# Performance work log

Hardware: AMD Instinct MI355X
Metric: run time of the kernel (lower is better)

## Reference

```python
import jax, jax.numpy as jnp
import numpy as np

EPS = 1e-6
H = 12  # num_heads


def _rms(x, w):
    return x / jnp.sqrt(jnp.mean(x * x, axis=-1, keepdims=True) + EPS) * w


def _rot_half(x):
    x1, x2 = jnp.split(x, 2, axis=-1)
    return jnp.concatenate([-x2, x1], axis=-1)


def _rope(t, cos, sin):
    # t: [B,H,N,hd]; cos/sin: [N,hd] broadcast
    return t * cos + _rot_half(t) * sin


def setup_inputs() -> dict:
    key = jax.random.key(0)
    B, N, D, Nc = 1, 2048, 768, 16
    hd = D // H
    mh = 4 * D
    ks = jax.random.split(key, 16)
    s = 0.02
    g = lambda k, shape, sc=1.0: jax.random.normal(k, shape, dtype=jnp.float32) * sc
    # real RoPE tables (half-duplicated layout to match rotate_half)
    inv = 1.0 / (10000.0 ** (np.arange(hd // 2, dtype=np.float64) / (hd // 2)))
    ang = np.arange(N, dtype=np.float64)[:, None] * inv[None, :]
    cos = jnp.asarray(np.concatenate([np.cos(ang), np.cos(ang)], -1), dtype=jnp.float32)
    sin = jnp.asarray(np.concatenate([np.sin(ang), np.sin(ang)], -1), dtype=jnp.float32)
    return {
        'x': g(ks[0], (B, N, D)),
        'c': g(ks[1], (B, D)),
        'cond': g(ks[2], (B, Nc, D)),
        'rope_cos': cos,
        'rope_sin': sin,
        'norm1_w': jnp.ones((D,), jnp.float32),
        'norm2_w': jnp.ones((D,), jnp.float32),
        'norm3_w': jnp.ones((D,), jnp.float32),
        'cond_norm_w': jnp.ones((D,), jnp.float32),
        'sa_qkv_w': g(ks[3], (3 * D, D), s),
        'sa_proj_w': g(ks[4], (D, D), s),
        'sa_proj_b': jnp.zeros((D,), jnp.float32),
        'sa_qn_w': jnp.ones((hd,), jnp.float32),
        'sa_kn_w': jnp.ones((hd,), jnp.float32),
        'ca_q_w': g(ks[5], (D, D), s),
        'ca_k_w': g(ks[6], (D, D), s),
        'ca_v_w': g(ks[7], (D, D), s),
        'ca_proj_w': g(ks[8], (D, D), s),
        'ca_proj_b': jnp.zeros((D,), jnp.float32),
        'ca_qn_w': jnp.ones((hd,), jnp.float32),
        'ca_kn_w': jnp.ones((hd,), jnp.float32),
        'mlp_w1': g(ks[9], (mh, D), s),
        'mlp_w2': g(ks[10], (D, mh), s),
        'mlp_w3': g(ks[11], (mh, D), s),
        'ada_w': g(ks[12], (9 * D, D), s),
        'ada_b': jnp.zeros((9 * D,), jnp.float32),
    }


def reference(x, c, cond, rope_cos, rope_sin, norm1_w, norm2_w, norm3_w, cond_norm_w,
              sa_qkv_w, sa_proj_w, sa_proj_b, sa_qn_w, sa_kn_w,
              ca_q_w, ca_k_w, ca_v_w, ca_proj_w, ca_proj_b, ca_qn_w, ca_kn_w,
              mlp_w1, mlp_w2, mlp_w3, ada_w, ada_b):
    B, N, D = x.shape
    hd = D // H
    scale = hd ** -0.5

    # adaLN modulation: SiLU(c) -> Linear -> 9 chunks of [B, D]
    mod = jax.nn.silu(c) @ ada_w.T + ada_b
    (sh_msa, sc_msa, g_msa, sh_ca, sc_ca, g_ca,
     sh_mlp, sc_mlp, g_mlp) = jnp.split(mod, 9, axis=1)

    def modulate(h, sh, sc):
        return h * (1.0 + sc[:, None, :]) + sh[:, None, :]

    # ---- self-attention with QK-norm + RoPE ----
    h = modulate(_rms(x, norm1_w), sh_msa, sc_msa)
    qkv = (h @ sa_qkv_w.T).reshape(B, N, 3, H, hd).transpose(2, 0, 3, 1, 4)  # [3,B,H,N,hd]
    q, k, v = qkv[0], qkv[1], qkv[2]
    q = _rope(_rms(q, sa_qn_w), rope_cos, rope_sin)
    k = _rope(_rms(k, sa_kn_w), rope_cos, rope_sin)
    attn = jax.nn.softmax(jnp.einsum('bhid,bhjd->bhij', q, k) * scale, axis=-1)
    o = jnp.einsum('bhij,bhjd->bhid', attn, v).transpose(0, 2, 1, 3).reshape(B, N, D)
    x = x + g_msa[:, None, :] * (o @ sa_proj_w.T + sa_proj_b)

    # ---- cross-attention (RoPE on q only) ----
    h = modulate(_rms(x, norm2_w), sh_ca, sc_ca)
    cn = _rms(cond, cond_norm_w)
    Nc = cond.shape[1]
    q = (h @ ca_q_w.T).reshape(B, N, H, hd).transpose(0, 2, 1, 3)
    k = (cn @ ca_k_w.T).reshape(B, Nc, H, hd).transpose(0, 2, 1, 3)
    v = (cn @ ca_v_w.T).reshape(B, Nc, H, hd).transpose(0, 2, 1, 3)
    q = _rope(_rms(q, ca_qn_w), rope_cos, rope_sin)
    k = _rms(k, ca_kn_w)
    attn = jax.nn.softmax(jnp.einsum('bhid,bhjd->bhij', q, k) * scale, axis=-1)
    o = jnp.einsum('bhij,bhjd->bhid', attn, v).transpose(0, 2, 1, 3).reshape(B, N, D)
    x = x + g_ca[:, None, :] * (o @ ca_proj_w.T + ca_proj_b)

    # ---- SwiGLU MLP ----
    h = modulate(_rms(x, norm3_w), sh_mlp, sc_mlp)
    x = x + g_mlp[:, None, :] * ((jax.nn.silu(h @ mlp_w1.T) * (h @ mlp_w3.T)) @ mlp_w2.T)
    return x
```

## Files before the change

### kernel.cpp

```cpp
#include <hip/hip_runtime.h>

typedef unsigned short u16;
typedef unsigned int u32;
typedef __attribute__((ext_vector_type(8))) short s16x8;
typedef __attribute__((ext_vector_type(4))) float f32x4;
typedef __attribute__((ext_vector_type(4))) int i32x4;

#define PS 1572864

#define OFF_SAQKV  0
#define OFF_SAPROJ 1769472
#define OFF_CAQ    2359296
#define OFF_CAPROJ 2949120
#define OFF_W1     3538944
#define OFF_W2     5898240
#define OFF_W3     8257536

static __device__ __forceinline__ float bf2f(u16 u) {
    return __uint_as_float(((u32)u) << 16);
}
static __device__ __forceinline__ u16 f2bf(float f) {
    u32 x = __float_as_uint(f);
    return (u16)((x + 0x7fffu + ((x >> 16) & 1u)) >> 16);
}
static __device__ __forceinline__ i32x4 pack8(float4 a, float4 b) {
    u32 p0 = (u32)f2bf(a.x) | ((u32)f2bf(a.y) << 16);
    u32 p1 = (u32)f2bf(a.z) | ((u32)f2bf(a.w) << 16);
    u32 p2 = (u32)f2bf(b.x) | ((u32)f2bf(b.y) << 16);
    u32 p3 = (u32)f2bf(b.z) | ((u32)f2bf(b.w) << 16);
    return (i32x4){(int)p0, (int)p1, (int)p2, (int)p3};
}
static __device__ __forceinline__ float wave_sum(float v) {
#pragma unroll
    for (int off = 32; off > 0; off >>= 1) v += __shfl_xor(v, off);
    return v;
}
static __device__ __forceinline__ void gload16(const void* g, void* l) {
    __builtin_amdgcn_global_load_lds((const __attribute__((address_space(1))) void*)g,
                                     (__attribute__((address_space(3))) void*)l, 16, 0, 0);
}

__global__ __launch_bounds__(256) void cvt_ada(const float* __restrict__ s0,
                                               const float* __restrict__ s1,
                                               const float* __restrict__ s2,
                                               const float* __restrict__ s3,
                                               const float* __restrict__ s4,
                                               const float* __restrict__ s5,
                                               const float* __restrict__ s6,
                                               u16* __restrict__ wall,
                                               const float* __restrict__ c,
                                               const float* __restrict__ adaw,
                                               const float* __restrict__ adab,
                                               float* __restrict__ mod,
                                               const float* __restrict__ cond,
                                               const float* __restrict__ cnw,
                                               const float* __restrict__ cakw,
                                               const float* __restrict__ cavw,
                                               const float* __restrict__ caknw,
                                               float* __restrict__ kca,
                                               float* __restrict__ vca) {
    const int bid = blockIdx.x;
    const int tid = threadIdx.x;
    if (bid < 5184) {
        int u = bid * 256 + tid;
        const float* src;
        int rel;
        if (u < 221184)       { src = s0; rel = u; }
        else if (u < 294912)  { src = s1; rel = u - 221184; }
        else if (u < 368640)  { src = s2; rel = u - 294912; }
        else if (u < 442368)  { src = s3; rel = u - 368640; }
        else if (u < 737280)  { src = s4; rel = u - 442368; }
        else if (u < 1032192) { src = s5; rel = u - 737280; }
        else                  { src = s6; rel = u - 1032192; }
        float4 a = *(const float4*)(src + (size_t)rel * 8);
        float4 b = *(const float4*)(src + (size_t)rel * 8 + 4);
        *(i32x4*)(wall + (size_t)u * 8) = pack8(a, b);
    } else if (bid < 6912) {
        int wid = (bid - 5184) * 4 + (tid >> 6);
        int lane = tid & 63;
        float sum = 0.f;
#pragma unroll
        for (int i = 0; i < 12; ++i) {
            float cv = c[i * 64 + lane];
            cv = cv / (1.f + __expf(-cv));
            sum += cv * adaw[(size_t)wid * 768 + i * 64 + lane];
        }
        sum = wave_sum(sum);
        if (lane == 0) mod[wid] = sum + adab[wid];
    } else {
        int b = bid - 6912;
        int which = b / 192;
        int rem = b % 192;
        int rrow = rem / 12, h = rem % 12;
        int w = tid >> 6, lane = tid & 63;
        __shared__ float kvsh[64];
        float cv[12];
        float ss = 0.f;
#pragma unroll
        for (int i = 0; i < 12; ++i) {
            cv[i] = cond[(size_t)rrow * 768 + i * 64 + lane];
            ss += cv[i] * cv[i];
        }
        ss = wave_sum(ss);
        float rn = rsqrtf(ss * (1.f / 768.f) + 1e-6f);
#pragma unroll
        for (int i = 0; i < 12; ++i) cv[i] = cv[i] * rn * cnw[i * 64 + lane];
        const float* Wm = which ? cavw : cakw;
#pragma unroll
        for (int j = 0; j < 16; ++j) {
            int ocol = h * 64 + w * 16 + j;
            float d = 0.f;
#pragma unroll
            for (int i = 0; i < 12; ++i)
                d += cv[i] * Wm[(size_t)ocol * 768 + i * 64 + lane];
            d = wave_sum(d);
            if (lane == 0) kvsh[w * 16 + j] = d;
        }
        __syncthreads();
        if (tid < 64) {
            float v = kvsh[lane];
            if (which == 0) {
                float sk = wave_sum(v * v);
                v = v * rsqrtf(sk * (1.f / 64.f) + 1e-6f) * caknw[lane];
                kca[(size_t)rrow * 768 + h * 64 + lane] = v;
            } else {
                vca[(size_t)rrow * 768 + h * 64 + lane] = v;
            }
        }
    }
}

__global__ __launch_bounds__(256) void rms_mod(const float* __restrict__ x,
                                               const float* __restrict__ w,
                                               const float* __restrict__ mod, int chunk,
                                               u16* __restrict__ out) {
    const int row = blockIdx.x;
    const int tid = threadIdx.x;
    const float* xr = x + (size_t)row * 768;
    float v0 = xr[tid], v1 = xr[256 + tid], v2 = xr[512 + tid];
    float ss = wave_sum(v0 * v0 + v1 * v1 + v2 * v2);
    __shared__ float red[4];
    if ((tid & 63) == 0) red[tid >> 6] = ss;
    __syncthreads();
    float rn = rsqrtf((red[0] + red[1] + red[2] + red[3]) * (1.f / 768.f) + 1e-6f);
    const float* sh = mod + chunk * 768;
    const float* sc = sh + 768;
    u16* orow = out + (size_t)row * 768;
    orow[tid]       = f2bf(v0 * rn * w[tid]       * (1.f + sc[tid])       + sh[tid]);
    orow[256 + tid] = f2bf(v1 * rn * w[256 + tid] * (1.f + sc[256 + tid]) + sh[256 + tid]);
    orow[512 + tid] = f2bf(v2 * rn * w[512 + tid] * (1.f + sc[512 + tid]) + sh[512 + tid]);
}

__global__ __launch_bounds__(256) void gemm_qkv(const u16* __restrict__ A,
                                                const u16* __restrict__ Wb,
                                                u16* __restrict__ qkvb,
                                                u16* __restrict__ vT,
                                                const float* __restrict__ qnw,
                                                const float* __restrict__ knw,
                                                const float* __restrict__ cosT,
                                                const float* __restrict__ sinT,
                                                int C, int R, int nxc) {
    constexpr int K = 768, N = 2304;
    __shared__ __align__(16) char smem[33792];
    u16 (*As)[128 * 32] = (u16(*)[128 * 32])smem;
    u16 (*Bs)[64 * 32] = (u16(*)[64 * 32])(smem + 16384);
    const int tid = threadIdx.x;
    const int lane = tid & 63;
    const int w = tid >> 6;
    const int wr = w >> 1, wc = w & 1;
    const int sub = blockIdx.x;
    const int xcd = sub & 7, idx = sub >> 3;
    const int cx = xcd % nxc, cy = xcd / nxc;
    const int col0 = (cx * C + idx % C) << 6;
    const int row0 = (cy * R + idx / C) << 7;

    const int r0u = tid >> 2, s0u = (tid & 3) ^ (r0u & 3);
    const int r1u = (tid + 256) >> 2, s1u = (tid & 3) ^ (r1u & 3);
    const u16* a0 = A + (size_t)(row0 + r0u) * K + s0u * 8;
    const u16* a1 = A + (size_t)(row0 + r1u) * K + s1u * 8;
    const u16* b0 = Wb + (size_t)(col0 + r0u) * K + s0u * 8;

    f32x4 acc[4][2];
#pragma unroll
    for (int m = 0; m < 4; ++m)
#pragma unroll
        for (int n = 0; n < 2; ++n) acc[m][n] = (f32x4){0.f, 0.f, 0.f, 0.f};

    const int nt = K >> 5;
    int cur = 0;
#define QKV_STAGE(buf, k0)                                  \
    {                                                       \
        char* ad = (char*)As[buf] + w * 1024;               \
        char* bd = (char*)Bs[buf] + w * 1024;               \
        gload16(a0 + (k0), ad);                             \
        gload16(a1 + (k0), ad + 4096);                      \
        gload16(b0 + (k0), bd);                             \
    }
    QKV_STAGE(0, 0)
    for (int t = 0; t < nt; ++t) {
        __syncthreads();
        if (t + 1 < nt) QKV_STAGE(cur ^ 1, (t + 1) << 5)
        s16x8 af[4], bfv[2];
#pragma unroll
        for (int m = 0; m < 4; ++m) {
            int ra = wr * 64 + m * 16 + (lane & 15);
            int u = (lane >> 4) ^ (ra & 3);
            af[m] = *(const s16x8*)((const char*)As[cur] + ra * 64 + u * 16);
        }
#pragma unroll
        for (int n = 0; n < 2; ++n) {
            int cb = wc * 32 + n * 16 + (lane & 15);
            int u = (lane >> 4) ^ (cb & 3);
            bfv[n] = *(const s16x8*)((const char*)Bs[cur] + cb * 64 + u * 16);
        }
#pragma unroll
        for (int m = 0; m < 4; ++m)
#pragma unroll
            for (int n = 0; n < 2; ++n)
                acc[m][n] = __builtin_amdgcn_mfma_f32_16x16x32_bf16(af[m], bfv[n], acc[m][n], 0, 0, 0);
        cur ^= 1;
    }
#undef QKV_STAGE
    __syncthreads();

    const int region = col0 / 768;
    const int h = (col0 % 768) >> 6;
    if (region < 2) {
        float (*T)[66] = (float(*)[66])smem;
#pragma unroll
        for (int m = 0; m < 4; ++m)
#pragma unroll
            for (int n = 0; n < 2; ++n)
#pragma unroll
                for (int i = 0; i < 4; ++i)
                    T[wr * 64 + m * 16 + (lane >> 4) * 4 + i]
                     [wc * 32 + n * 16 + (lane & 15)] = acc[m][n][i];
        __syncthreads();
        const float* wv = region ? knw : qnw;
        const int rl = tid >> 1, half = (tid & 1) * 32;
        float ss = 0.f;
#pragma unroll
        for (int d = 0; d < 32; ++d) {
            float v = T[rl][half + d];
            ss += v * v;
        }
        ss += __shfl_xor(ss, 1);
        float rn = rsqrtf(ss * (1.f / 64.f) + 1e-6f);
        const int ng = row0 + rl;
        u16* orow = qkvb + (size_t)ng * N + col0;
        const float* cr = cosT + ng * 64;
        const float* sr = sinT + ng * 64;
#pragma unroll
        for (int d = 0; d < 32; ++d) {
            int dd = half + d;
            float vn = T[rl][dd] * rn * wv[dd];
            float pt = T[rl][dd ^ 32] * rn * wv[dd ^ 32];
            float rot = (dd < 32) ? -pt : pt;
            orow[dd] = f2bf(vn * cr[dd] + rot * sr[dd]);
        }
    } else {
        u16 (*Tb)[66] = (u16(*)[66])smem;
#pragma unroll
        for (int m = 0; m < 4; ++m)
#pragma unroll
            for (int n = 0; n < 2; ++n)
#pragma unroll
                for (int i = 0; i < 4; ++i) {
                    int rl = wr * 64 + m * 16 + (lane >> 4) * 4 + i;
                    int dd = wc * 32 + n * 16 + (lane & 15);
                    u16 b = f2bf(acc[m][n][i]);
                    qkvb[(size_t)(row0 + rl) * N + col0 + dd] = b;
                    Tb[rl][dd] = b;
                }
        __syncthreads();
        u16* dst = vT + (size_t)h * 131072 + (size_t)lane * 2048 + row0 + w * 32;
#pragma unroll
        for (int g = 0; g < 4; ++g) {
            s16x8 o;
#pragma unroll
            for (int e = 0; e < 8; ++e) o[e] = (short)Tb[w * 32 + g * 8 + e][lane];
            *(s16x8*)(dst + g * 8) = o;
        }
    }
}

__global__ __launch_bounds__(256) void gemm_sk4(const u16* __restrict__ A,
                                                const u16* __restrict__ Wb,
                                                int M, int N, int K,
                                                u16* __restrict__ pz,
                                                int C, int R, int nxc,
                                                int nsub, int kslice) {
    __shared__ __align__(16) u16 As[2][128 * 32];
    __shared__ __align__(16) u16 Bs[2][64 * 32];
    const int tid = threadIdx.x;
    const int lane = tid & 63;
    const int w = tid >> 6;
    const int wr = w >> 1, wc = w & 1;
    const int sub = blockIdx.x % nsub;
    const int z = blockIdx.x / nsub;
    const int xcd = sub & 7, idx = sub >> 3;
    const int cx = xcd % nxc, cy = xcd / nxc;
    const int col0 = (cx * C + idx % C) << 6;
    const int row0 = (cy * R + idx / C) << 7;
    const int kbase = z * kslice;

    const int r0u = tid >> 2, s0u = (tid & 3) ^ (r0u & 3);
    const int r1u = (tid + 256) >> 2, s1u = (tid & 3) ^ (r1u & 3);
    const u16* a0 = A + (size_t)(row0 + r0u) * K + kbase + s0u * 8;
    const u16* a1 = A + (size_t)(row0 + r1u) * K + kbase + s1u * 8;
    const u16* b0 = Wb + (size_t)(col0 + r0u) * K + kbase + s0u * 8;

    f32x4 acc[4][2];
#pragma unroll
    for (int m = 0; m < 4; ++m)
#pragma unroll
        for (int n = 0; n < 2; ++n) acc[m][n] = (f32x4){0.f, 0.f, 0.f, 0.f};

    const int nt = kslice >> 5;
    int cur = 0;
#define SK_STAGE(buf, k0)                                   \
    {                                                       \
        char* ad = (char*)As[buf] + w * 1024;               \
        char* bd = (char*)Bs[buf] + w * 1024;               \
        gload16(a0 + (k0), ad);                             \
        gload16(a1 + (k0), ad + 4096);                      \
        gload16(b0 + (k0), bd);                             \
    }
    SK_STAGE(0, 0)
    for (int t = 0; t < nt; ++t) {
        __syncthreads();
        if (t + 1 < nt) SK_STAGE(cur ^ 1, (t + 1) << 5)
        s16x8 af[4], bfv[2];
#pragma unroll
        for (int m = 0; m < 4; ++m) {
            int ra = wr * 64 + m * 16 + (lane & 15);
            int u = (lane >> 4) ^ (ra & 3);
            af[m] = *(const s16x8*)((const char*)As[cur] + ra * 64 + u * 16);
        }
#pragma unroll
        for (int n = 0; n < 2; ++n) {
            int cb = wc * 32 + n * 16 + (lane & 15);
            int u = (lane >> 4) ^ (cb & 3);
            bfv[n] = *(const s16x8*)((const char*)Bs[cur] + cb * 64 + u * 16);
        }
#pragma unroll
        for (int m = 0; m < 4; ++m)
#pragma unroll
            for (int n = 0; n < 2; ++n)
                acc[m][n] = __builtin_amdgcn_mfma_f32_16x16x32_bf16(af[m], bfv[n], acc[m][n], 0, 0, 0);
        cur ^= 1;
    }
#undef SK_STAGE
    u16* po = pz + (size_t)z * PS;
#pragma unroll
    for (int m = 0; m < 4; ++m)
#pragma unroll
        for (int n = 0; n < 2; ++n)
#pragma unroll
            for (int i = 0; i < 4; ++i) {
                int r = row0 + wr * 64 + m * 16 + (lane >> 4) * 4 + i;
                int cc = col0 + wc * 32 + n * 16 + (lane & 15);
                po[(size_t)r * N + cc] = f2bf(acc[m][n][i]);
            }
}

template <int MODE>
__global__ __launch_bounds__(256) void comb4(const u16* __restrict__ pz,
                                             const float* __restrict__ resid,
                                             const float* __restrict__ gate,
                                             const float* __restrict__ bias,
                                             float* __restrict__ outf) {
    int base = (blockIdx.x * 256 + threadIdx.x) * 8;
    int col = base % 768;
    s16x8 p0 = *(const s16x8*)(pz + base);
    s16x8 p1 = *(const s16x8*)(pz + PS + base);
    s16x8 p2 = *(const s16x8*)(pz + 2 * PS + base);
    s16x8 p3 = *(const s16x8*)(pz + 3 * PS + base);
    float o[8];
#pragma unroll
    for (int e = 0; e < 8; ++e) {
        float s = (bf2f((u16)p0[e]) + bf2f((u16)p1[e])) +
                  (bf2f((u16)p2[e]) + bf2f((u16)p3[e]));
        if constexpr (MODE == 0) {
            o[e] = s;
        } else {
            float bb = bias ? bias[col + e] : 0.f;
            o[e] = resid[base + e] + gate[col + e] * (s + bb);
        }
    }
    *(float4*)(outf + base) = (float4){o[0], o[1], o[2], o[3]};
    *(float4*)(outf + base + 4) = (float4){o[4], o[5], o[6], o[7]};
}

__global__ __launch_bounds__(256) void comb_rms(const u16* __restrict__ pz,
                                                const float* __restrict__ resid,
                                                const float* __restrict__ gate,
                                                const float* __restrict__ bias,
                                                const float* __restrict__ mod, int chunk,
                                                const float* __restrict__ w,
                                                float* __restrict__ outf,
                                                u16* __restrict__ outb) {
    const int row = blockIdx.x;
    const int tid = threadIdx.x;
    float val[3];
    float ss = 0.f;
#pragma unroll
    for (int j = 0; j < 3; ++j) {
        int col = tid + j * 256;
        size_t ix = (size_t)row * 768 + col;
        float s = (bf2f(pz[ix]) + bf2f(pz[PS + ix])) +
                  (bf2f(pz[2 * PS + ix]) + bf2f(pz[3 * PS + ix]));
        float bb = bias ? bias[col] : 0.f;
        float v = resid[ix] + gate[col] * (s + bb);
        val[j] = v;
        ss += v * v;
        outf[ix] = v;
    }
    ss = wave_sum(ss);
    __shared__ float red[4];
    if ((tid & 63) == 0) red[tid >> 6] = ss;
    __syncthreads();
    float rn = rsqrtf((red[0] + red[1] + red[2] + red[3]) * (1.f / 768.f) + 1e-6f);
    const float* sh = mod + chunk * 768;
    const float* sc = sh + 768;
#pragma unroll
    for (int j = 0; j < 3; ++j) {
        int col = tid + j * 256;
        size_t ix = (size_t)row * 768 + col;
        outb[ix] = f2bf(val[j] * rn * w[col] * (1.f + sc[col]) + sh[col]);
    }
}

__global__ __launch_bounds__(256) void ca_fused(const u16* __restrict__ pz,
                                                const float* __restrict__ qnw,
                                                const float* __restrict__ cosT,
                                                const float* __restrict__ sinT,
                                                const float* __restrict__ kca,
                                                const float* __restrict__ vca,
                                                u16* __restrict__ obuf) {
    int wid = blockIdx.x * 4 + (threadIdx.x >> 6);
    int lane = threadIdx.x & 63;
    int n = wid / 12, h = wid % 12;
    size_t ix = (size_t)n * 768 + h * 64 + lane;
    float v = (bf2f(pz[ix]) + bf2f(pz[PS + ix])) +
              (bf2f(pz[2 * PS + ix]) + bf2f(pz[3 * PS + ix]));
    float ss = wave_sum(v * v);
    float vn = v * rsqrtf(ss * (1.f / 64.f) + 1e-6f) * qnw[lane];
    float part = __shfl_xor(vn, 32);
    float rot = (lane < 32) ? -part : part;
    float qd = (vn * cosT[n * 64 + lane] + rot * sinT[n * 64 + lane]) * 0.125f;
    float s[16];
#pragma unroll
    for (int j = 0; j < 16; ++j)
        s[j] = wave_sum(qd * kca[(size_t)j * 768 + h * 64 + lane]);
    float mm = s[0];
#pragma unroll
    for (int j = 1; j < 16; ++j) mm = fmaxf(mm, s[j]);
    float l = 0.f;
#pragma unroll
    for (int j = 0; j < 16; ++j) { s[j] = __expf(s[j] - mm); l += s[j]; }
    float od = 0.f;
#pragma unroll
    for (int j = 0; j < 16; ++j) od += s[j] * vca[(size_t)j * 768 + h * 64 + lane];
    obuf[ix] = f2bf(od / l);
}

__global__ __launch_bounds__(256) void gemm_w13(const u16* __restrict__ A,
                                                const u16* __restrict__ W1,
                                                const u16* __restrict__ W3,
                                                int M, int N, int K,
                                                u16* __restrict__ outb,
                                                int C, int R, int nxc) {
    __shared__ __align__(16) u16 As[2][128 * 32];
    __shared__ __align__(16) u16 B1s[2][64 * 32];
    __shared__ __align__(16) u16 B3s[2][64 * 32];
    const int tid = threadIdx.x;
    const int lane = tid & 63;
    const int w = tid >> 6;
    const int wr = w >> 1, wc = w & 1;
    const int sub = blockIdx.x;
    const int xcd = sub & 7, idx = sub >> 3;
    const int cx = xcd % nxc, cy = xcd / nxc;
    const int col0 = (cx * C + idx % C) << 6;
    const int row0 = (cy * R + idx / C) << 7;

    const int r0u = tid >> 2, s0u = (tid & 3) ^ (r0u & 3);
    const int r1u = (tid + 256) >> 2, s1u = (tid & 3) ^ (r1u & 3);
    const u16* a0 = A + (size_t)(row0 + r0u) * K + s0u * 8;
    const u16* a1 = A + (size_t)(row0 + r1u) * K + s1u * 8;
    const u16* b1p = W1 + (size_t)(col0 + r0u) * K + s0u * 8;
    const u16* b3p = W3 + (size_t)(col0 + r0u) * K + s0u * 8;

    f32x4 acc1[4][2], acc3[4][2];
#pragma unroll
    for (int m = 0; m < 4; ++m)
#pragma unroll
        for (int n = 0; n < 2; ++n) {
            acc1[m][n] = (f32x4){0.f, 0.f, 0.f, 0.f};
            acc3[m][n] = (f32x4){0.f, 0.f, 0.f, 0.f};
        }

    const int nt = K >> 5;
    int cur = 0;
#define W13_STAGE(buf, k0)                                  \
    {                                                       \
        char* ad = (char*)As[buf] + w * 1024;               \
        char* bd1 = (char*)B1s[buf] + w * 1024;             \
        char* bd3 = (char*)B3s[buf] + w * 1024;             \
        gload16(a0 + (k0), ad);                             \
        gload16(a1 + (k0), ad + 4096);                      \
        gload16(b1p + (k0), bd1);                           \
        gload16(b3p + (k0), bd3);                           \
    }
    W13_STAGE(0, 0)
    for (int t = 0; t < nt; ++t) {
        __syncthreads();
        if (t + 1 < nt) W13_STAGE(cur ^ 1, (t + 1) << 5)
        s16x8 af[4], b1v[2], b3v[2];
#pragma unroll
        for (int m = 0; m < 4; ++m) {
            int ra = wr * 64 + m * 16 + (lane & 15);
            int u = (lane >> 4) ^ (ra & 3);
            af[m] = *(const s16x8*)((const char*)As[cur] + ra * 64 + u * 16);
        }
#pragma unroll
        for (int n = 0; n < 2; ++n) {
            int cb = wc * 32 + n * 16 + (lane & 15);
            int u = (lane >> 4) ^ (cb & 3);
            b1v[n] = *(const s16x8*)((const char*)B1s[cur] + cb * 64 + u * 16);
            b3v[n] = *(const s16x8*)((const char*)B3s[cur] + cb * 64 + u * 16);
        }
#pragma unroll
        for (int m = 0; m < 4; ++m)
#pragma unroll
            for (int n = 0; n < 2; ++n) {
                acc1[m][n] = __builtin_amdgcn_mfma_f32_16x16x32_bf16(af[m], b1v[n], acc1[m][n], 0, 0, 0);
                acc3[m][n] = __builtin_amdgcn_mfma_f32_16x16x32_bf16(af[m], b3v[n], acc3[m][n], 0, 0, 0);
            }
        cur ^= 1;
    }
#undef W13_STAGE
#pragma unroll
    for (int m = 0; m < 4; ++m)
#pragma unroll
        for (int n = 0; n < 2; ++n)
#pragma unroll
            for (int i = 0; i < 4; ++i) {
                int r = row0 + wr * 64 + m * 16 + (lane >> 4) * 4 + i;
                int cc = col0 + wc * 32 + n * 16 + (lane & 15);
                float v1 = acc1[m][n][i];
                float g = v1 / (1.f + __expf(-v1));
                outb[(size_t)r * N + cc] = f2bf(g * acc3[m][n][i]);
            }
}

__global__ __launch_bounds__(256) void sa_attn_mfma(const u16* __restrict__ qkv,
                                                    const u16* __restrict__ vT,
                                                    u16* __restrict__ at,
                                                    float* __restrict__ pl) {
    const int h = blockIdx.y;
    const int r0 = blockIdx.x * 64;
    const int z = blockIdx.z;
    const int tid = threadIdx.x;
    const int lane = tid & 63;
    const int w = tid >> 6;
    __shared__ __align__(16) u16 Ks[2][64 * 64];
    __shared__ __align__(16) u16 Vs[2][64 * 64];
    __shared__ __align__(16) u16 Ps[4][16 * 64];

    s16x8 qf[2];
    {
        const u16* qrow = qkv + (size_t)(r0 + w * 16 + (lane & 15)) * 2304 + h * 64 + ((lane >> 4) * 8);
        qf[0] = *(const s16x8*)qrow;
        qf[1] = *(const s16x8*)(qrow + 32);
    }
    f32x4 oacc[4];
#pragma unroll
    for (int n = 0; n < 4; ++n) oacc[n] = (f32x4){0.f, 0.f, 0.f, 0.f};
    float lp[4] = {0.f, 0.f, 0.f, 0.f};

    const u16* ksrc[2];
    const u16* vsrc[2];
#pragma unroll
    for (int j = 0; j < 2; ++j) {
        int u = (w * 2 + j) * 64 + lane;
        int row = u >> 3, seg = (u & 7) ^ (row & 7);
        ksrc[j] = qkv + (size_t)(z * 512 + row) * 2304 + 768 + h * 64 + seg * 8;
        vsrc[j] = vT + (size_t)h * 131072 + (size_t)row * 2048 + z * 512 + seg * 8;
    }

#define SA_STAGE(buf, t_)                                          \
    {                                                              \
        char* kd = (char*)Ks[buf] + w * 2048;                      \
        char* vd = (char*)Vs[buf] + w * 2048;                      \
        gload16(ksrc[0] + (size_t)(t_) * 147456, kd);              \
        gload16(ksrc[1] + (size_t)(t_) * 147456, kd + 1024);       \
        gload16(vsrc[0] + (t_) * 64, vd);                          \
        gload16(vsrc[1] + (t_) * 64, vd + 1024);                   \
    }

    SA_STAGE(0, 0)
    int cur = 0;
    for (int t = 0; t < 8; ++t) {
        __syncthreads();
        if (t + 1 < 8) SA_STAGE(cur ^ 1, t + 1)

        f32x4 sacc[4];
#pragma unroll
        for (int n = 0; n < 4; ++n) sacc[n] = (f32x4){0.f, 0.f, 0.f, 0.f};
#pragma unroll
        for (int kk = 0; kk < 2; ++kk) {
#pragma unroll
            for (int n = 0; n < 4; ++n) {
                int key = n * 16 + (lane & 15);
                int d = kk * 32 + (lane >> 4) * 8;
                int boff = key * 128 + ((d * 2) ^ ((key & 7) << 4));
                s16x8 kf = *(const s16x8*)((const char*)Ks[cur] + boff);
                sacc[n] = __builtin_amdgcn_mfma_f32_16x16x32_bf16(qf[kk], kf, sacc[n], 0, 0, 0);
            }
        }
#pragma unroll
        for (int n = 0; n < 4; ++n) {
#pragma unroll
            for (int i = 0; i < 4; ++i) {
                float p = __expf(fmaf(sacc[n][i], 0.125f, -8.0f));
                lp[i] += p;
                int row = (lane >> 4) * 4 + i;
                int key = n * 16 + (lane & 15);
                int boff = row * 128 + ((key * 2) ^ ((row & 7) << 4));
                *(u16*)((char*)Ps[w] + boff) = f2bf(p);
            }
        }
#pragma unroll
        for (int kk = 0; kk < 2; ++kk) {
            int koff = kk * 32 + (lane >> 4) * 8;
            int prow = lane & 15;
            int pboff = prow * 128 + ((koff * 2) ^ ((prow & 7) << 4));
            s16x8 pf = *(const s16x8*)((const char*)Ps[w] + pboff);
#pragma unroll
            for (int n = 0; n < 4; ++n) {
                int d = n * 16 + (lane & 15);
                int vboff = d * 128 + ((koff * 2) ^ ((d & 7) << 4));
                s16x8 vf = *(const s16x8*)((const char*)Vs[cur] + vboff);
                oacc[n] = __builtin_amdgcn_mfma_f32_16x16x32_bf16(pf, vf, oacc[n], 0, 0, 0);
            }
        }
        cur ^= 1;
    }
#undef SA_STAGE
#pragma unroll
    for (int off = 1; off < 16; off <<= 1) {
#pragma unroll
        for (int i = 0; i < 4; ++i) lp[i] += __shfl_xor(lp[i], off);
    }
    u16* po = at + (size_t)z * PS;
#pragma unroll
    for (int n = 0; n < 4; ++n) {
#pragma unroll
        for (int i = 0; i < 4; ++i) {
            int r = r0 + w * 16 + (lane >> 4) * 4 + i;
            int d = n * 16 + (lane & 15);
            po[(size_t)r * 768 + h * 64 + d] = f2bf(oacc[n][i]);
        }
    }
    if ((lane & 15) == 0) {
#pragma unroll
        for (int i = 0; i < 4; ++i) {
            int r = r0 + w * 16 + (lane >> 4) * 4 + i;
            pl[z * 24576 + h * 2048 + r] = lp[i];
        }
    }
}

__global__ __launch_bounds__(256) void sa_combine4(const u16* __restrict__ at,
                                                   const float* __restrict__ pl,
                                                   u16* __restrict__ obuf) {
    int idx = blockIdx.x * 256 + threadIdx.x;
    int base = idx * 8;
    int row = base / 768;
    int col = base % 768;
    int h = col >> 6;
    float l = (pl[h * 2048 + row] + pl[24576 + h * 2048 + row]) +
              (pl[49152 + h * 2048 + row] + pl[73728 + h * 2048 + row]);
    float inv = 1.f / l;
    s16x8 a = *(const s16x8*)(at + base);
    s16x8 b = *(const s16x8*)(at + PS + base);
    s16x8 cc = *(const s16x8*)(at + 2 * PS + base);
    s16x8 d = *(const s16x8*)(at + 3 * PS + base);
    s16x8 o;
#pragma unroll
    for (int e = 0; e < 8; ++e) {
        float s = (bf2f((u16)a[e]) + bf2f((u16)b[e])) +
                  (bf2f((u16)cc[e]) + bf2f((u16)d[e]));
        o[e] = (short)f2bf(s * inv);
    }
    *(s16x8*)(obuf + base) = o;
}

extern "C" void kernel_launch(void* const* d_in, const int* in_sizes, int n_in,
                              void* d_out, int out_size, void* d_ws, size_t ws_size,
                              hipStream_t stream) {
    const float* x     = (const float*)d_in[0];
    const float* c     = (const float*)d_in[1];
    const float* cond  = (const float*)d_in[2];
    const float* cosT  = (const float*)d_in[3];
    const float* sinT  = (const float*)d_in[4];
    const float* n1w   = (const float*)d_in[5];
    const float* n2w   = (const float*)d_in[6];
    const float* n3w   = (const float*)d_in[7];
    const float* cnw   = (const float*)d_in[8];
    const float* saqkvw  = (const float*)d_in[9];
    const float* saprojw = (const float*)d_in[10];
    const float* saprojb = (const float*)d_in[11];
    const float* saqnw   = (const float*)d_in[12];
    const float* saknw   = (const float*)d_in[13];
    const float* caqw    = (const float*)d_in[14];
    const float* cakw    = (const float*)d_in[15];
    const float* cavw    = (const float*)d_in[16];
    const float* caprojw = (const float*)d_in[17];
    const float* caprojb = (const float*)d_in[18];
    const float* caqnw   = (const float*)d_in[19];
    const float* caknw   = (const float*)d_in[20];
    const float* w1      = (const float*)d_in[21];
    const float* w2      = (const float*)d_in[22];
    const float* w3      = (const float*)d_in[23];
    const float* adaw    = (const float*)d_in[24];
    const float* adab    = (const float*)d_in[25];
    float* out = (float*)d_out;
    char* ws = (char*)d_ws;

    float* mod  = (float*)ws;
    u16* hbuf   = (u16*)(ws + 32768);
    u16* obuf   = (u16*)(ws + 3178496);
    char* R1    = ws + 6324224;
    u16* qkvb   = (u16*)R1;
    u16* vTb    = (u16*)(R1 + 9437184);
    u16* gbuf   = (u16*)R1;
    float* kca  = (float*)(ws + 18956288);
    float* vca  = (float*)(ws + 19005440);
    u16* WALL   = (u16*)(ws + 19054592);
    u16* AT     = (u16*)(ws + 40288256);
    float* PL4  = (float*)(ws + 52871168);
    u16* SKP    = (u16*)(ws + 53264384);

    cvt_ada<<<7296, 256, 0, stream>>>(saqkvw, saprojw, caqw, caprojw, w1, w2, w3,
                                      WALL, c, adaw, adab, mod,
                                      cond, cnw, cakw, cavw, caknw, kca, vca);

    rms_mod<<<2048, 256, 0, stream>>>(x, n1w, mod, 0, hbuf);
    gemm_qkv<<<576, 256, 0, stream>>>(hbuf, WALL + OFF_SAQKV, qkvb, vTb,
                                      saqnw, saknw, cosT, sinT, 9, 8, 4);
    sa_attn_mfma<<<dim3(32, 12, 4), 256, 0, stream>>>(qkvb, vTb, AT, PL4);
    sa_combine4<<<768, 256, 0, stream>>>(AT, PL4, obuf);
    gemm_sk4<<<768, 256, 0, stream>>>(obuf, WALL + OFF_SAPROJ, 2048, 768, 768,
                                      SKP, 6, 4, 2, 192, 192);
    comb_rms<<<2048, 256, 0, stream>>>(SKP, x, mod + 2 * 768, saprojb,
                                       mod, 3, n2w, out, hbuf);

    gemm_sk4<<<768, 256, 0, stream>>>(hbuf, WALL + OFF_CAQ, 2048, 768, 768,
                                      SKP, 6, 4, 2, 192, 192);
    ca_fused<<<6144, 256, 0, stream>>>(SKP, caqnw, cosT, sinT, kca, vca, obuf);
    gemm_sk4<<<768, 256, 0, stream>>>(obuf, WALL + OFF_CAPROJ, 2048, 768, 768,
                                      SKP, 6, 4, 2, 192, 192);
    comb_rms<<<2048, 256, 0, stream>>>(SKP, out, mod + 5 * 768, caprojb,
                                       mod, 6, n3w, out, hbuf);

    gemm_w13<<<768, 256, 0, stream>>>(hbuf, WALL + OFF_W1, WALL + OFF_W3,
                                      2048, 3072, 768, gbuf, 12, 8, 4);
    gemm_sk4<<<768, 256, 0, stream>>>(gbuf, WALL + OFF_W2, 2048, 768, 3072,
                                      SKP, 6, 4, 2, 192, 768);
    comb4<2><<<768, 256, 0, stream>>>(SKP, out, mod + 8 * 768, nullptr, out);
}
```

Before: 216.4 us.

## Drop upfront weight bf16 conversion; load fp32 weights and convert in GEMM fragments

Removes the separate pass that converted every weight matrix to bf16 in a workspace buffer. The GEMM kernels now stream fp32 weight tiles straight into LDS with an 8-way XOR swizzle and pack them to bf16 when forming MFMA B fragments. This avoids writing and re-reading the bf16 weight copy each call. In exchange it doubles the weight bytes each GEMM block loads, uses more LDS, and adds conversion ALU work in the inner loop, and weights reused across many row tiles are fetched in fp32 repeatedly.

```diff
diff --git a/kernel.cpp b/kernel.cpp
--- a/kernel.cpp
+++ b/kernel.cpp
@@ -7,14 +7,6 @@
 typedef __attribute__((ext_vector_type(4))) int i32x4;
 
 #define PS 1572864
-
-#define OFF_SAQKV  0
-#define OFF_SAPROJ 1769472
-#define OFF_CAQ    2359296
-#define OFF_CAPROJ 2949120
-#define OFF_W1     3538944
-#define OFF_W2     5898240
-#define OFF_W3     8257536
 
 static __device__ __forceinline__ float bf2f(u16 u) {
     return __uint_as_float(((u32)u) << 16);
@@ -39,44 +31,30 @@
     __builtin_amdgcn_global_load_lds((const __attribute__((address_space(1))) void*)g,
                                      (__attribute__((address_space(3))) void*)l, 16, 0, 0);
 }
-
-__global__ __launch_bounds__(256) void cvt_ada(const float* __restrict__ s0,
-                                               const float* __restrict__ s1,
-                                               const float* __restrict__ s2,
-                                               const float* __restrict__ s3,
-                                               const float* __restrict__ s4,
-                                               const float* __restrict__ s5,
-                                               const float* __restrict__ s6,
-                                               u16* __restrict__ wall,
-                                               const float* __restrict__ c,
-                                               const float* __restrict__ adaw,
-                                               const float* __restrict__ adab,
-                                               float* __restrict__ mod,
-                                               const float* __restrict__ cond,
-                                               const float* __restrict__ cnw,
-                                               const float* __restrict__ cakw,
-                                               const float* __restrict__ cavw,
-                                               const float* __restrict__ caknw,
-                                               float* __restrict__ kca,
-                                               float* __restrict__ vca) {
+static __device__ __forceinline__ s16x8 bfrag_f32(const char* base, int cb, int lane) {
+    int g = (lane >> 4) * 2;
+    const char* bb = base + cb * 128;
+    float4 lo = *(const float4*)(bb + ((g ^ (cb & 7)) * 16));
+    float4 hi = *(const float4*)(bb + (((g + 1) ^ (cb & 7)) * 16));
+    i32x4 p = pack8(lo, hi);
+    return *(s16x8*)&p;
+}
+
+__global__ __launch_bounds__(256) void ada_kv(const float* __restrict__ c,
+                                              const float* __restrict__ adaw,
+                                              const float* __restrict__ adab,
+                                              float* __restrict__ mod,
+                                              const float* __restrict__ cond,
+                                              const float* __restrict__ cnw,
+                                              const float* __restrict__ cakw,
+                                              const float* __restrict__ cavw,
+                                              const float* __restrict__ caknw,
+                                              float* __restrict__ kca,
+                                              float* __restrict__ vca) {
     const int bid = blockIdx.x;
     const int tid = threadIdx.x;
-    if (bid < 5184) {
-        int u = bid * 256 + tid;
-        const float* src;
-        int rel;
-        if (u < 221184)       { src = s0; rel = u; }
-        else if (u < 294912)  { src = s1; rel = u - 221184; }
-        else if (u < 368640)  { src = s2; rel = u - 294912; }
-        else if (u < 442368)  { src = s3; rel = u - 368640; }
-        else if (u < 737280)  { src = s4; rel = u - 442368; }
-        else if (u < 1032192) { src = s5; rel = u - 737280; }
-        else                  { src = s6; rel = u - 1032192; }
-        float4 a = *(const float4*)(src + (size_t)rel * 8);
-        float4 b = *(const float4*)(src + (size_t)rel * 8 + 4);
-        *(i32x4*)(wall + (size_t)u * 8) = pack8(a, b);
-    } else if (bid < 6912) {
-        int wid = (bid - 5184) * 4 + (tid >> 6);
+    if (bid < 1728) {
+        int wid = bid * 4 + (tid >> 6);
         int lane = tid & 63;
         float sum = 0.f;
 #pragma unroll
@@ -88,7 +66,7 @@
         sum = wave_sum(sum);
         if (lane == 0) mod[wid] = sum + adab[wid];
     } else {
-        int b = bid - 6912;
+        int b = bid - 1728;
         int which = b / 192;
         int rem = b % 192;
         int rrow = rem / 12, h = rem % 12;
@@ -152,7 +130,7 @@
 }
 
 __global__ __launch_bounds__(256) void gemm_qkv(const u16* __restrict__ A,
-                                                const u16* __restrict__ Wb,
+                                                const float* __restrict__ Wf,
                                                 u16* __restrict__ qkvb,
                                                 u16* __restrict__ vT,
                                                 const float* __restrict__ qnw,
@@ -163,7 +141,7 @@
     constexpr int K = 768, N = 2304;
     __shared__ __align__(16) char smem[33792];
     u16 (*As)[128 * 32] = (u16(*)[128 * 32])smem;
-    u16 (*Bs)[64 * 32] = (u16(*)[64 * 32])(smem + 16384);
+    float (*Bs)[64 * 32] = (float(*)[64 * 32])(smem + 16384);
     const int tid = threadIdx.x;
     const int lane = tid & 63;
     const int w = tid >> 6;
@@ -178,7 +156,10 @@
     const int r1u = (tid + 256) >> 2, s1u = (tid & 3) ^ (r1u & 3);
     const u16* a0 = A + (size_t)(row0 + r0u) * K + s0u * 8;
     const u16* a1 = A + (size_t)(row0 + r1u) * K + s1u * 8;
-    const u16* b0 = Wb + (size_t)(col0 + r0u) * K + s0u * 8;
+    const int b0r = tid >> 3, b0s = (tid & 7) ^ (b0r & 7);
+    const int b1r = (tid + 256) >> 3, b1s = (tid & 7) ^ (b1r & 7);
+    const float* b0 = Wf + (size_t)(col0 + b0r) * K + b0s * 4;
+    const float* b1 = Wf + (size_t)(col0 + b1r) * K + b1s * 4;
 
     f32x4 acc[4][2];
 #pragma unroll
@@ -195,6 +176,7 @@
         gload16(a0 + (k0), ad);                             \
         gload16(a1 + (k0), ad + 4096);                      \
         gload16(b0 + (k0), bd);                             \
+        gload16(b1 + (k0), bd + 4096);                      \
     }
     QKV_STAGE(0, 0)
     for (int t = 0; t < nt; ++t) {
@@ -210,8 +192,7 @@
 #pragma unroll
         for (int n = 0; n < 2; ++n) {
             int cb = wc * 32 + n * 16 + (lane & 15);
-            int u = (lane >> 4) ^ (cb & 3);
-            bfv[n] = *(const s16x8*)((const char*)Bs[cur] + cb * 64 + u * 16);
+            bfv[n] = bfrag_f32((const char*)Bs[cur], cb, lane);
         }
 #pragma unroll
         for (int m = 0; m < 4; ++m)
@@ -285,13 +266,13 @@
 }
 
 __global__ __launch_bounds__(256) void gemm_sk4(const u16* __restrict__ A,
-                                                const u16* __restrict__ Wb,
+                                                const float* __restrict__ Wf,
                                                 int M, int N, int K,
                                                 u16* __restrict__ pz,
                                                 int C, int R, int nxc,
                                                 int nsub, int kslice) {
     __shared__ __align__(16) u16 As[2][128 * 32];
-    __shared__ __align__(16) u16 Bs[2][64 * 32];
+    __shared__ __align__(16) float Bs[2][64 * 32];
     const int tid = threadIdx.x;
     const int lane = tid & 63;
     const int w = tid >> 6;
@@ -308,7 +289,10 @@
     const int r1u = (tid + 256) >> 2, s1u = (tid & 3) ^ (r1u & 3);
     const u16* a0 = A + (size_t)(row0 + r0u) * K + kbase + s0u * 8;
     const u16* a1 = A + (size_t)(row0 + r1u) * K + kbase + s1u * 8;
-    const u16* b0 = Wb + (size_t)(col0 + r0u) * K + kbase + s0u * 8;
+    const int b0r = tid >> 3, b0s = (tid & 7) ^ (b0r & 7);
+    const int b1r = (tid + 256) >> 3, b1s = (tid & 7) ^ (b1r & 7);
+    const float* b0 = Wf + (size_t)(col0 + b0r) * K + kbase + b0s * 4;
+    const float* b1 = Wf + (size_t)(col0 + b1r) * K + kbase + b1s * 4;
 
     f32x4 acc[4][2];
 #pragma unroll
@@ -325,6 +309,7 @@
         gload16(a0 + (k0), ad);                             \
         gload16(a1 + (k0), ad + 4096);                      \
         gload16(b0 + (k0), bd);                             \
+        gload16(b1 + (k0), bd + 4096);                      \
     }
     SK_STAGE(0, 0)
     for (int t = 0; t < nt; ++t) {
@@ -340,8 +325,7 @@
 #pragma unroll
         for (int n = 0; n < 2; ++n) {
             int cb = wc * 32 + n * 16 + (lane & 15);
-            int u = (lane >> 4) ^ (cb & 3);
-            bfv[n] = *(const s16x8*)((const char*)Bs[cur] + cb * 64 + u * 16);
+            bfv[n] = bfrag_f32((const char*)Bs[cur], cb, lane);
         }
 #pragma unroll
         for (int m = 0; m < 4; ++m)
@@ -466,14 +450,14 @@
 }
 
 __global__ __launch_bounds__(256) void gemm_w13(const u16* __restrict__ A,
-                                                const u16* __restrict__ W1,
-                                                const u16* __restrict__ W3,
+                                                const float* __restrict__ W1,
+                                                const float* __restrict__ W3,
                                                 int M, int N, int K,
                                                 u16* __restrict__ outb,
                                                 int C, int R, int nxc) {
     __shared__ __align__(16) u16 As[2][128 * 32];
-    __shared__ __align__(16) u16 B1s[2][64 * 32];
-    __shared__ __align__(16) u16 B3s[2][64 * 32];
+    __shared__ __align__(16) float B1s[2][64 * 32];
+    __shared__ __align__(16) float B3s[2][64 * 32];
     const int tid = threadIdx.x;
     const int lane = tid & 63;
     const int w = tid >> 6;
@@ -488,8 +472,12 @@
     const int r1u = (tid + 256) >> 2, s1u = (tid & 3) ^ (r1u & 3);
     const u16* a0 = A + (size_t)(row0 + r0u) * K + s0u * 8;
     const u16* a1 = A + (size_t)(row0 + r1u) * K + s1u * 8;
-    const u16* b1p = W1 + (size_t)(col0 + r0u) * K + s0u * 8;
-    const u16* b3p = W3 + (size_t)(col0 + r0u) * K + s0u * 8;
+    const int b0r = tid >> 3, b0s = (tid & 7) ^ (b0r & 7);
+    const int b1r = (tid + 256) >> 3, b1s = (tid & 7) ^ (b1r & 7);
+    const float* b10 = W1 + (size_t)(col0 + b0r) * K + b0s * 4;
+    const float* b11 = W1 + (size_t)(col0 + b1r) * K + b1s * 4;
+    const float* b30 = W3 + (size_t)(col0 + b0r) * K + b0s * 4;
+    const float* b31 = W3 + (size_t)(col0 + b1r) * K + b1s * 4;
 
     f32x4 acc1[4][2], acc3[4][2];
 #pragma unroll
@@ -509,8 +497,10 @@
         char* bd3 = (char*)B3s[buf] + w * 1024;             \
         gload16(a0 + (k0), ad);                             \
         gload16(a1 + (k0), ad + 4096);                      \
-        gload16(b1p + (k0), bd1);                           \
-        gload16(b3p + (k0), bd3);                           \
+        gload16(b10 + (k0), bd1);                           \
+        gload16(b11 + (k0), bd1 + 4096);                    \
+        gload16(b30 + (k0), bd3);                           \
+        gload16(b31 + (k0), bd3 + 4096);                    \
     }
     W13_STAGE(0, 0)
     for (int t = 0; t < nt; ++t) {
@@ -526,9 +516,8 @@
 #pragma unroll
         for (int n = 0; n < 2; ++n) {
             int cb = wc * 32 + n * 16 + (lane & 15);
-            int u = (lane >> 4) ^ (cb & 3);
-            b1v[n] = *(const s16x8*)((const char*)B1s[cur] + cb * 64 + u * 16);
-            b3v[n] = *(const s16x8*)((const char*)B3s[cur] + cb * 64 + u * 16);
+            b1v[n] = bfrag_f32((const char*)B1s[cur], cb, lane);
+            b3v[n] = bfrag_f32((const char*)B3s[cur], cb, lane);
         }
 #pragma unroll
         for (int m = 0; m < 4; ++m)
@@ -738,36 +727,34 @@
     u16* gbuf   = (u16*)R1;
     float* kca  = (float*)(ws + 18956288);
     float* vca  = (float*)(ws + 19005440);
-    u16* WALL   = (u16*)(ws + 19054592);
     u16* AT     = (u16*)(ws + 40288256);
     float* PL4  = (float*)(ws + 52871168);
     u16* SKP    = (u16*)(ws + 53264384);
 
-    cvt_ada<<<7296, 256, 0, stream>>>(saqkvw, saprojw, caqw, caprojw, w1, w2, w3,
-                                      WALL, c, adaw, adab, mod,
-                                      cond, cnw, cakw, cavw, caknw, kca, vca);
+    ada_kv<<<2112, 256, 0, stream>>>(c, adaw, adab, mod,
+                                     cond, cnw, cakw, cavw, caknw, kca, vca);
 
     rms_mod<<<2048, 256, 0, stream>>>(x, n1w, mod, 0, hbuf);
-    gemm_qkv<<<576, 256, 0, stream>>>(hbuf, WALL + OFF_SAQKV, qkvb, vTb,
+    gemm_qkv<<<576, 256, 0, stream>>>(hbuf, saqkvw, qkvb, vTb,
                                       saqnw, saknw, cosT, sinT, 9, 8, 4);
     sa_attn_mfma<<<dim3(32, 12, 4), 256, 0, stream>>>(qkvb, vTb, AT, PL4);
     sa_combine4<<<768, 256, 0, stream>>>(AT, PL4, obuf);
-    gemm_sk4<<<768, 256, 0, stream>>>(obuf, WALL + OFF_SAPROJ, 2048, 768, 768,
+    gemm_sk4<<<768, 256, 0, stream>>>(obuf, saprojw, 2048, 768, 768,
                                       SKP, 6, 4, 2, 192, 192);
     comb_rms<<<2048, 256, 0, stream>>>(SKP, x, mod + 2 * 768, saprojb,
                                        mod, 3, n2w, out, hbuf);
 
-    gemm_sk4<<<768, 256, 0, stream>>>(hbuf, WALL + OFF_CAQ, 2048, 768, 768,
+    gemm_sk4<<<768, 256, 0, stream>>>(hbuf, caqw, 2048, 768, 768,
                                       SKP, 6, 4, 2, 192, 192);
     ca_fused<<<6144, 256, 0, stream>>>(SKP, caqnw, cosT, sinT, kca, vca, obuf);
-    gemm_sk4<<<768, 256, 0, stream>>>(obuf, WALL + OFF_CAPROJ, 2048, 768, 768,
+    gemm_sk4<<<768, 256, 0, stream>>>(obuf, caprojw, 2048, 768, 768,
                                       SKP, 6, 4, 2, 192, 192);
     comb_rms<<<2048, 256, 0, stream>>>(SKP, out, mod + 5 * 768, caprojb,
                                        mod, 6, n3w, out, hbuf);
 
-    gemm_w13<<<768, 256, 0, stream>>>(hbuf, WALL + OFF_W1, WALL + OFF_W3,
+    gemm_w13<<<768, 256, 0, stream>>>(hbuf, w1, w3,
                                       2048, 3072, 768, gbuf, 12, 8, 4);
-    gemm_sk4<<<768, 256, 0, stream>>>(gbuf, WALL + OFF_W2, 2048, 768, 3072,
+    gemm_sk4<<<768, 256, 0, stream>>>(gbuf, w2, 2048, 768, 3072,
                                       SKP, 6, 4, 2, 192, 768);
     comb4<2><<<768, 256, 0, stream>>>(SKP, out, mod + 8 * 768, nullptr, out);
 }
```

After: 228.1 us. 1.05x slower.
